# Kernel optimization log

Hardware: AMD Instinct MI355X
Metric: run time of the kernel (lower is better)

The kernel has to match this reference:

```python
import jax, jax.numpy as jnp
import numpy as np

N = 100000      # nodes
E = 1600000     # edges (avg degree 16)
F_NODE = 128
F_EDGE = 32
H = 32          # hidden size hard-coded in module


def setup_inputs() -> dict:
    key = jax.random.key(0)
    ks = jax.random.split(key, 16)
    w = lambda k, s: jax.random.normal(k, s, jnp.float32) * 0.05
    z = lambda n: jnp.zeros((n,), jnp.float32)
    return {
        "x": jax.random.normal(ks[0], (N, F_NODE), jnp.float32),
        "edge_index": jax.random.randint(ks[1], (2, E), 0, N),
        "edge_attr": jax.random.normal(ks[2], (E, F_EDGE), jnp.float32),
        "W_node": w(ks[3], (F_NODE, H)), "b_node": z(H),
        "W_edge": w(ks[4], (F_EDGE, H)), "b_edge": z(H),
        # TGCN: three GCNConv(32,32) gate convs + three Linear(64,32)
        "Wg_z": w(ks[5], (H, H)), "bg_z": z(H),
        "Wg_r": w(ks[6], (H, H)), "bg_r": z(H),
        "Wg_h": w(ks[7], (H, H)), "bg_h": z(H),
        "Wl_z": w(ks[8], (2 * H, H)), "bl_z": z(H),
        "Wl_r": w(ks[9], (2 * H, H)), "bl_r": z(H),
        "Wl_h": w(ks[10], (2 * H, H)), "bl_h": z(H),
        "W_out": w(ks[11], (3 * H, 1)), "b_out": z(1),
    }


def _gcn(x, row, col, dis, W, b, n):
    # GCNConv with added self-loops and symmetric normalization.
    xw = x @ W                                        # [N, H]
    msg = (dis[row] * dis[col])[:, None] * xw[row]    # [E, H]
    agg = jax.ops.segment_sum(msg, col, num_segments=n)
    agg = agg + (dis * dis)[:, None] * xw             # self-loop term
    return agg + b


def reference(x, edge_index, edge_attr, W_node, b_node, W_edge, b_edge,
              Wg_z, bg_z, Wg_r, bg_r, Wg_h, bg_h,
              Wl_z, bl_z, Wl_r, bl_r, Wl_h, bl_h, W_out, b_out):
    n = x.shape[0]
    row, col = edge_index[0], edge_index[1]
    x_enc = jax.nn.relu(x @ W_node + b_node)          # [N, 32]
    e_enc = jax.nn.relu(edge_attr @ W_edge + b_edge)  # [E, 32]

    # degree (target side) including self loop
    deg = jax.ops.segment_sum(jnp.ones_like(col, dtype=x.dtype), col,
                              num_segments=n) + 1.0
    dis = jax.lax.rsqrt(deg)

    h0 = jnp.zeros_like(x_enc)                        # TGCN initial state H=None -> zeros
    Z = jax.nn.sigmoid(
        jnp.concatenate([_gcn(x_enc, row, col, dis, Wg_z, bg_z, n), h0], 1) @ Wl_z + bl_z)
    R = jax.nn.sigmoid(
        jnp.concatenate([_gcn(x_enc, row, col, dis, Wg_r, bg_r, n), h0], 1) @ Wl_r + bl_r)
    Ht = jnp.tanh(
        jnp.concatenate([_gcn(x_enc, row, col, dis, Wg_h, bg_h, n), h0 * R], 1) @ Wl_h + bl_h)
    h = Z * h0 + (1.0 - Z) * Ht                       # [N, 32]

    # edge-level gather-concat + final linear -> [E, 1]
    edge_feat = jnp.concatenate([h[row], h[col], e_enc], axis=1)  # [E, 96]
    return edge_feat @ W_out + b_out
```

## Files before the change

kernel.cpp:

```cpp
#include <hip/hip_runtime.h>
#include <hip/hip_bf16.h>

#define F_NODE 128
#define BINCAP 64

typedef float f32x4 __attribute__((ext_vector_type(4)));
typedef float f32x2 __attribute__((ext_vector_type(2)));

__device__ __forceinline__ float bflo(unsigned int v) {
    return __uint_as_float(v << 16);
}
__device__ __forceinline__ float bfhi(unsigned int v) {
    return __uint_as_float(v & 0xffff0000u);
}

__global__ void k_prep(const float* __restrict__ Wn,
                       const float* __restrict__ Wgz, const float* __restrict__ Wgh,
                       const float* __restrict__ Wlz, const float* __restrict__ Wlh,
                       const float* __restrict__ bgz, const float* __restrict__ bgh,
                       const float* __restrict__ blz, const float* __restrict__ blh,
                       const float* __restrict__ We,
                       float* __restrict__ Wnt, float* __restrict__ M2,
                       float* __restrict__ cvec, float* __restrict__ Wet,
                       int* __restrict__ cursor, int N) {
    int tid = threadIdx.x;
    int t = blockIdx.x * 256 + tid;
    int gstride = gridDim.x * 256;
    for (int j = t; j < N; j += gstride) cursor[j] = 0;

    if (blockIdx.x != 0) return;
    for (int j = tid; j < 32 * 128; j += 256) {
        int f = j >> 7, k = j & 127;
        Wnt[j] = Wn[k * 32 + f];
    }
    for (int j = tid; j < 32 * 64; j += 256) {
        int k = j >> 6, g = j & 63, f = g & 31;
        const float* G = (g < 32) ? Wgz : Wgh;
        const float* L = (g < 32) ? Wlz : Wlh;
        float s = 0.f;
        for (int q = 0; q < 32; ++q) s += G[k * 32 + q] * L[q * 32 + f];
        M2[j] = s;
    }
    for (int j = tid; j < 64; j += 256) {
        int f = j & 31;
        const float* L  = (j < 32) ? Wlz : Wlh;
        const float* bg = (j < 32) ? bgz : bgh;
        const float* bl = (j < 32) ? blz : blh;
        float s = bl[f];
        for (int q = 0; q < 32; ++q) s += bg[q] * L[q * 32 + f];
        cvec[j] = s;
    }
    for (int j = tid; j < 32 * 32; j += 256) {
        int f = j >> 5, k = j & 31;
        Wet[j] = We[k * 32 + f];
    }
}

__global__ __launch_bounds__(256) void k_fatm(
        const int* __restrict__ row, const int* __restrict__ col,
        int* __restrict__ cursor, int* __restrict__ bin,
        const float* __restrict__ ea, const float* __restrict__ Wet,
        const float* __restrict__ be, const float* __restrict__ Wout,
        const float* __restrict__ bout, float* __restrict__ out, int E) {
    __shared__ float sW[1024];
    __shared__ float sb[32], sw3[32];
    int tid = threadIdx.x;
    for (int j = tid; j < 1024; j += 256) sW[j] = Wet[j];
    if (tid < 32) { sb[tid] = be[tid]; sw3[tid] = Wout[64 + tid]; }
    __syncthreads();

    int e = blockIdx.x * 256 + tid;
    if (e >= E) return;

    int c = col[e];
    int r = row[e];
    const f32x4* erow = (const f32x4*)(ea + (size_t)e * 32);
    f32x4 er[8];
    #pragma unroll
    for (int k = 0; k < 8; ++k) er[k] = erow[k];

    int pos = atomicAdd(&cursor[c], 1);

    float p = 0.f;
    #pragma unroll 4
    for (int f = 0; f < 32; ++f) {
        const f32x4* wf = (const f32x4*)(sW + f * 32);
        f32x4 v0 = er[0] * wf[0];
        f32x4 v1 = er[1] * wf[1];
        #pragma unroll
        for (int k = 2; k < 8; k += 2) {
            v0 += er[k] * wf[k];
            v1 += er[k + 1] * wf[k + 1];
        }
        f32x4 v = v0 + v1;
        float sfin = (v[0] + v[1]) + (v[2] + v[3]);
        p += fmaxf(sb[f] + sfin, 0.f) * sw3[f];
    }
    out[e] = p + bout[0];
    if (pos < BINCAP) bin[((size_t)c << 6) + pos] = r;
}

__global__ __launch_bounds__(256) void k_enc(
        const float* __restrict__ x, const float* __restrict__ bn,
        const float* __restrict__ Wnt, const int* __restrict__ cursor,
        __hip_bfloat16* __restrict__ ysb, int N) {
    __shared__ float sx[4][128];
    int tid = threadIdx.x;
    int w = tid >> 6, l = tid & 63;
    int f = l & 31, kh = l >> 5;

    f32x4 wreg[16];
    const f32x4* wp = (const f32x4*)(Wnt + f * 128 + kh * 64);
    #pragma unroll
    for (int r = 0; r < 16; ++r) wreg[r] = wp[r];
    float bnf = bn[f];

    int stride = gridDim.x * 4;
    int i = blockIdx.x * 4 + w;
    f32x2 xv = {0.f, 0.f};
    if (i < N) xv = ((const f32x2*)(x + (size_t)i * F_NODE))[l];

    for (; i < N; i += stride) {
        sx[w][2 * l]     = xv[0];
        sx[w][2 * l + 1] = xv[1];
        int inext = i + stride;
        if (inext < N)
            xv = ((const f32x2*)(x + (size_t)inext * F_NODE))[l];

        const f32x4* sxp = (const f32x4*)(&sx[w][kh * 64]);
        f32x4 a0 = sxp[0] * wreg[0];
        f32x4 a1 = sxp[1] * wreg[1];
        f32x4 a2 = sxp[2] * wreg[2];
        f32x4 a3 = sxp[3] * wreg[3];
        #pragma unroll
        for (int r = 4; r < 16; r += 4) {
            a0 += sxp[r]     * wreg[r];
            a1 += sxp[r + 1] * wreg[r + 1];
            a2 += sxp[r + 2] * wreg[r + 2];
            a3 += sxp[r + 3] * wreg[r + 3];
        }
        f32x4 av = (a0 + a1) + (a2 + a3);
        float acc = (av[0] + av[1]) + (av[2] + av[3]);
        acc += __shfl_xor(acc, 32);
        float d = rsqrtf((float)cursor[i] + 1.0f);
        acc = d * fmaxf(acc + bnf, 0.f);
        if (l < 32)
            ysb[(size_t)i * 32 + f] = __float2bfloat16(acc);
    }
}

__global__ __launch_bounds__(256) void k_gather(
        const int* __restrict__ cursor, const int* __restrict__ bin,
        const unsigned short* __restrict__ ysb,
        const float* __restrict__ M2, const float* __restrict__ cvec,
        const float* __restrict__ Wout,
        float* __restrict__ hr, float* __restrict__ hc, int N) {
    int tid = threadIdx.x;
    int w = tid >> 6, l = tid & 63;
    int q = l & 7, s = l >> 3;

    float mcol[32];
    #pragma unroll
    for (int k = 0; k < 32; ++k) mcol[k] = M2[k * 64 + l];
    float cvl = cvec[l];
    float w0l = Wout[l & 31];
    float w1l = Wout[32 + (l & 31)];

    int stride = gridDim.x * 4;
    for (int c = blockIdx.x * 4 + w; c < N; c += stride) {
        int truec = cursor[c];
        float dc = rsqrtf((float)truec + 1.0f);
        int cnt = truec < BINCAP ? truec : BINCAP;
        const int* bp = bin + ((size_t)c << 6);
        int myr = (l < cnt) ? bp[l] : 0;

        float a0 = 0.f, a1 = 0.f, a2 = 0.f, a3 = 0.f;
        uint2 sv = *(const uint2*)(ysb + (size_t)c * 32 + 4 * q);
        if (s == 0) {
            a0 = bflo(sv.x); a1 = bfhi(sv.x);
            a2 = bflo(sv.y); a3 = bfhi(sv.y);
        }
        for (int j = 0; j < cnt; j += 8) {
            int jj = j + s;
            if (jj < cnt) {
                int r = __shfl(myr, jj);
                uint2 v = *(const uint2*)(ysb + (size_t)r * 32 + 4 * q);
                a0 += bflo(v.x); a1 += bfhi(v.x);
                a2 += bflo(v.y); a3 += bfhi(v.y);
            }
        }
        a0 += __shfl_xor(a0, 8);  a1 += __shfl_xor(a1, 8);
        a2 += __shfl_xor(a2, 8);  a3 += __shfl_xor(a3, 8);
        a0 += __shfl_xor(a0, 16); a1 += __shfl_xor(a1, 16);
        a2 += __shfl_xor(a2, 16); a3 += __shfl_xor(a3, 16);
        a0 += __shfl_xor(a0, 32); a1 += __shfl_xor(a1, 32);
        a2 += __shfl_xor(a2, 32); a3 += __shfl_xor(a3, 32);

        float acc = 0.f;
        #pragma unroll
        for (int kq = 0; kq < 8; ++kq) {
            float s0 = __shfl(a0, kq), t1 = __shfl(a1, kq);
            float t2 = __shfl(a2, kq), t3 = __shfl(a3, kq);
            acc += s0 * mcol[4 * kq]     + t1 * mcol[4 * kq + 1]
                 + t2 * mcol[4 * kq + 2] + t3 * mcol[4 * kq + 3];
        }
        float a = dc * acc + cvl;
        float v = (l < 32) ? (1.f / (1.f + __expf(-a))) : tanhf(a);
        float o = __shfl_xor(v, 32);
        float h = (1.f - v) * o;
        float pr = h * w0l;
        float pc = h * w1l;
        #pragma unroll
        for (int m = 16; m >= 1; m >>= 1) {
            pr += __shfl_xor(pr, m);
            pc += __shfl_xor(pc, m);
        }
        if (l == 0) { hr[c] = pr; hc[c] = pc; }
    }
}

__global__ __launch_bounds__(256) void k_edge_add(
        const int* __restrict__ row, const int* __restrict__ col,
        const float* __restrict__ hr, const float* __restrict__ hc,
        float* __restrict__ out, int E) {
    int e = blockIdx.x * 256 + threadIdx.x;
    if (e < E) out[e] += hr[row[e]] + hc[col[e]];
}

extern "C" void kernel_launch(void* const* d_in, const int* in_sizes, int n_in,
                              void* d_out, int out_size, void* d_ws, size_t ws_size,
                              hipStream_t stream) {
    const float* x    = (const float*)d_in[0];
    const int*   ei   = (const int*)  d_in[1];
    const float* ea   = (const float*)d_in[2];
    const float* Wn   = (const float*)d_in[3];
    const float* bn   = (const float*)d_in[4];
    const float* We   = (const float*)d_in[5];
    const float* be   = (const float*)d_in[6];
    const float* Wgz  = (const float*)d_in[7];
    const float* bgz  = (const float*)d_in[8];
    const float* Wgh  = (const float*)d_in[11];
    const float* bgh  = (const float*)d_in[12];
    const float* Wlz  = (const float*)d_in[13];
    const float* blz  = (const float*)d_in[14];
    const float* Wlh  = (const float*)d_in[17];
    const float* blh  = (const float*)d_in[18];
    const float* Wout = (const float*)d_in[19];
    const float* bout = (const float*)d_in[20];

    int N = in_sizes[0] / F_NODE;
    int E = in_sizes[1] / 2;
    const int* row = ei;
    const int* col = ei + E;

    float* ws    = (float*)d_ws;
    __hip_bfloat16* ysb = (__hip_bfloat16*)ws;
    int*   bin   = (int*)(ws + (size_t)16 * N);
    float* Wnt   = ws + (size_t)80 * N;
    float* M2    = Wnt + 4096;
    float* Wet   = M2 + 2048;
    float* cvec  = Wet + 1024;
    float* hr    = cvec + 64;
    float* hc    = hr + N;
    int*   cursor= (int*)(hc + N);
    float* out   = (float*)d_out;

    k_prep<<<400, 256, 0, stream>>>(Wn, Wgz, Wgh, Wlz, Wlh, bgz, bgh, blz, blh,
                                    We, Wnt, M2, cvec, Wet, cursor, N);
    int eb = (E + 255) / 256;
    k_fatm<<<eb, 256, 0, stream>>>(row, col, cursor, bin, ea, Wet, be, Wout,
                                   bout, out, E);
    k_enc<<<768, 256, 0, stream>>>(x, bn, Wnt, cursor, ysb, N);
    k_gather<<<2048, 256, 0, stream>>>(cursor, bin, (const unsigned short*)ysb,
                                       M2, cvec, Wout, hr, hc, N);
    k_edge_add<<<eb, 256, 0, stream>>>(row, col, hr, hc, out, E);
}
```

Measured before the change: 246.1 us.

## Fuse node encoder into edge kernel and defer degree scaling to a separate pass

```diff
diff --git a/kernel.cpp b/kernel.cpp
--- a/kernel.cpp
+++ b/kernel.cpp
@@ -3,6 +3,7 @@
 
 #define F_NODE 128
 #define BINCAP 64
+#define ENCB 768
 
 typedef float f32x4 __attribute__((ext_vector_type(4)));
 typedef float f32x2 __attribute__((ext_vector_type(2)));
@@ -12,6 +13,10 @@
 }
 __device__ __forceinline__ float bfhi(unsigned int v) {
     return __uint_as_float(v & 0xffff0000u);
+}
+__device__ __forceinline__ unsigned bfpack(float f) {
+    __hip_bfloat16 b = __float2bfloat16(f);
+    return (unsigned)*reinterpret_cast<unsigned short*>(&b);
 }
 
 __global__ void k_prep(const float* __restrict__ Wn,
@@ -20,7 +25,7 @@
                        const float* __restrict__ bgz, const float* __restrict__ bgh,
                        const float* __restrict__ blz, const float* __restrict__ blh,
                        const float* __restrict__ We,
-                       float* __restrict__ Wnt, float* __restrict__ M2,
+                       unsigned* __restrict__ Wnp, float* __restrict__ M2,
                        float* __restrict__ cvec, float* __restrict__ Wet,
                        int* __restrict__ cursor, int N) {
     int tid = threadIdx.x;
@@ -29,9 +34,11 @@
     for (int j = t; j < N; j += gstride) cursor[j] = 0;
 
     if (blockIdx.x != 0) return;
-    for (int j = tid; j < 32 * 128; j += 256) {
-        int f = j >> 7, k = j & 127;
-        Wnt[j] = Wn[k * 32 + f];
+    for (int j = tid; j < 64 * 32; j += 256) {
+        int k2 = j >> 5, f = j & 31;
+        unsigned lo = bfpack(Wn[(2 * k2) * 32 + f]);
+        unsigned hi = bfpack(Wn[(2 * k2 + 1) * 32 + f]);
+        Wnp[j] = lo | (hi << 16);
     }
     for (int j = tid; j < 32 * 64; j += 256) {
         int k = j >> 6, g = j & 63, f = g & 31;
@@ -61,15 +68,51 @@
         int* __restrict__ cursor, int* __restrict__ bin,
         const float* __restrict__ ea, const float* __restrict__ Wet,
         const float* __restrict__ be, const float* __restrict__ Wout,
-        const float* __restrict__ bout, float* __restrict__ out, int E) {
-    __shared__ float sW[1024];
-    __shared__ float sb[32], sw3[32];
-    int tid = threadIdx.x;
+        const float* __restrict__ bout, float* __restrict__ out,
+        const float* __restrict__ x, const float* __restrict__ bn,
+        const unsigned* __restrict__ Wnp, __hip_bfloat16* __restrict__ ysb,
+        int E, int N) {
+    __shared__ unsigned smem[3104];
+    int bid = blockIdx.x, tid = threadIdx.x;
+
+    if (bid < ENCB) {
+        unsigned* sWnp = smem;
+        float*    sx   = (float*)(smem + 2048);
+        float*    sbn  = (float*)(smem + 3072);
+        for (int j = tid; j < 2048; j += 256) sWnp[j] = Wnp[j];
+        if (tid < 32) sbn[tid] = bn[tid];
+        __syncthreads();
+
+        int w = tid >> 6, l = tid & 63;
+        int f = l & 31, h2 = l >> 5;
+        float* sxw = sx + w * 256 + h2 * 128;
+
+        int NP = (N + 1) >> 1;
+        int stride = ENCB * 4;
+        for (int p = bid * 4 + w; p < NP; p += stride) {
+            int node = 2 * p + h2;
+            int nd = node < N ? node : N - 1;
+            ((f32x4*)sxw)[f] = ((const f32x4*)(x + (size_t)nd * F_NODE))[f];
+            float acc = sbn[f];
+            #pragma unroll 8
+            for (int k2 = 0; k2 < 64; ++k2) {
+                unsigned wv = sWnp[k2 * 32 + f];
+                acc += sxw[2 * k2] * bflo(wv) + sxw[2 * k2 + 1] * bfhi(wv);
+            }
+            if (node < N)
+                ysb[(size_t)node * 32 + f] = __float2bfloat16(fmaxf(acc, 0.f));
+        }
+        return;
+    }
+
+    float* sW  = (float*)smem;
+    float* sb  = (float*)(smem + 1024);
+    float* sw3 = (float*)(smem + 1056);
     for (int j = tid; j < 1024; j += 256) sW[j] = Wet[j];
     if (tid < 32) { sb[tid] = be[tid]; sw3[tid] = Wout[64 + tid]; }
     __syncthreads();
 
-    int e = blockIdx.x * 256 + tid;
+    int e = (bid - ENCB) * 256 + tid;
     if (e >= E) return;
 
     int c = col[e];
@@ -100,53 +143,21 @@
     if (pos < BINCAP) bin[((size_t)c << 6) + pos] = r;
 }
 
-__global__ __launch_bounds__(256) void k_enc(
-        const float* __restrict__ x, const float* __restrict__ bn,
-        const float* __restrict__ Wnt, const int* __restrict__ cursor,
-        __hip_bfloat16* __restrict__ ysb, int N) {
-    __shared__ float sx[4][128];
-    int tid = threadIdx.x;
-    int w = tid >> 6, l = tid & 63;
-    int f = l & 31, kh = l >> 5;
-
-    f32x4 wreg[16];
-    const f32x4* wp = (const f32x4*)(Wnt + f * 128 + kh * 64);
+__global__ __launch_bounds__(256) void k_scale(
+        uint4* __restrict__ ysb4, const int* __restrict__ cursor, int N) {
+    int t = blockIdx.x * 256 + threadIdx.x;
+    if (t >= N * 4) return;
+    float d = rsqrtf((float)cursor[t >> 2] + 1.0f);
+    uint4 v = ysb4[t];
+    unsigned in[4] = {v.x, v.y, v.z, v.w};
+    unsigned r[4];
     #pragma unroll
-    for (int r = 0; r < 16; ++r) wreg[r] = wp[r];
-    float bnf = bn[f];
-
-    int stride = gridDim.x * 4;
-    int i = blockIdx.x * 4 + w;
-    f32x2 xv = {0.f, 0.f};
-    if (i < N) xv = ((const f32x2*)(x + (size_t)i * F_NODE))[l];
-
-    for (; i < N; i += stride) {
-        sx[w][2 * l]     = xv[0];
-        sx[w][2 * l + 1] = xv[1];
-        int inext = i + stride;
-        if (inext < N)
-            xv = ((const f32x2*)(x + (size_t)inext * F_NODE))[l];
-
-        const f32x4* sxp = (const f32x4*)(&sx[w][kh * 64]);
-        f32x4 a0 = sxp[0] * wreg[0];
-        f32x4 a1 = sxp[1] * wreg[1];
-        f32x4 a2 = sxp[2] * wreg[2];
-        f32x4 a3 = sxp[3] * wreg[3];
-        #pragma unroll
-        for (int r = 4; r < 16; r += 4) {
-            a0 += sxp[r]     * wreg[r];
-            a1 += sxp[r + 1] * wreg[r + 1];
-            a2 += sxp[r + 2] * wreg[r + 2];
-            a3 += sxp[r + 3] * wreg[r + 3];
-        }
-        f32x4 av = (a0 + a1) + (a2 + a3);
-        float acc = (av[0] + av[1]) + (av[2] + av[3]);
-        acc += __shfl_xor(acc, 32);
-        float d = rsqrtf((float)cursor[i] + 1.0f);
-        acc = d * fmaxf(acc + bnf, 0.f);
-        if (l < 32)
-            ysb[(size_t)i * 32 + f] = __float2bfloat16(acc);
-    }
+    for (int j = 0; j < 4; ++j) {
+        unsigned lo = bfpack(bflo(in[j]) * d);
+        unsigned hi = bfpack(bfhi(in[j]) * d);
+        r[j] = lo | (hi << 16);
+    }
+    ysb4[t] = make_uint4(r[0], r[1], r[2], r[3]);
 }
 
 __global__ __launch_bounds__(256) void k_gather(
@@ -256,8 +267,8 @@
     float* ws    = (float*)d_ws;
     __hip_bfloat16* ysb = (__hip_bfloat16*)ws;
     int*   bin   = (int*)(ws + (size_t)16 * N);
-    float* Wnt   = ws + (size_t)80 * N;
-    float* M2    = Wnt + 4096;
+    unsigned* Wnp= (unsigned*)(ws + (size_t)80 * N);
+    float* M2    = ws + (size_t)80 * N + 2048;
     float* Wet   = M2 + 2048;
     float* cvec  = Wet + 1024;
     float* hr    = cvec + 64;
@@ -266,12 +277,13 @@
     float* out   = (float*)d_out;
 
     k_prep<<<400, 256, 0, stream>>>(Wn, Wgz, Wgh, Wlz, Wlh, bgz, bgh, blz, blh,
-                                    We, Wnt, M2, cvec, Wet, cursor, N);
+                                    We, Wnp, M2, cvec, Wet, cursor, N);
     int eb = (E + 255) / 256;
-    k_fatm<<<eb, 256, 0, stream>>>(row, col, cursor, bin, ea, Wet, be, Wout,
-                                   bout, out, E);
-    k_enc<<<768, 256, 0, stream>>>(x, bn, Wnt, cursor, ysb, N);
-    k_gather<<<2048, 256, 0, stream>>>(cursor, bin, (const unsigned short*)ysb,
+    k_fatm<<<ENCB + eb, 256, 0, stream>>>(row, col, cursor, bin, ea, Wet, be,
+                                          Wout, bout, out, x, bn, Wnp, ysb,
+                                          E, N);
+    k_scale<<<(4 * N + 255) / 256, 256, 0, stream>>>((uint4*)ysb, cursor, N);
+    k_gather<<<8192, 256, 0, stream>>>(cursor, bin, (const unsigned short*)ysb,
                                        M2, cvec, Wout, hr, hc, N);
     k_edge_add<<<eb, 256, 0, stream>>>(row, col, hr, hc, out, E);
 }
```

New measurement: 231.5 us. 1.06x faster.
